# Performance work log

Hardware: AMD Instinct MI355X
Metric: run time of the kernel (lower is better)

Reference implementation:

```python
import jax, jax.numpy as jnp
import numpy as np

C = 1.0  # curvature
EPS = 1e-5

@jax.custom_vjp
def arsinh(x):
    return jnp.log(jnp.maximum(x + jnp.sqrt(1.0 + x * x), 1e-5))

def _arsinh_fwd(x):
    return arsinh(x), x

def _arsinh_bwd(x, g):
    return (g / jnp.sqrt(1.0 + x * x),)

arsinh.defvjp(_arsinh_fwd, _arsinh_bwd)

def tanh_clamped(x, clamp=15.0):
    return jnp.tanh(jnp.clip(x, -clamp, clamp))

def expmap0(u, c):
    sqrt_c = c ** 0.5
    u_norm = jnp.maximum(jnp.linalg.norm(u, axis=-1, keepdims=True), 1e-5)
    return tanh_clamped(sqrt_c * u_norm) * u / (sqrt_c * u_norm)

def mobius_addition_batch(x, y, c):
    # x: [K, D], y: [N, D] -> [K, N, D]
    xy = jnp.einsum('kd,nd->kn', x, y)
    x2 = jnp.sum(x * x, axis=-1, keepdims=True)          # [K, 1]
    y2 = jnp.sum(y * y, axis=-1, keepdims=True)          # [N, 1]
    num = (1.0 + 2.0 * c * xy + c * y2.T)[:, :, None] * x[:, None, :]
    num = num + (1.0 - c * x2)[:, :, None] * y[None, :, :]
    denom = 1.0 + 2.0 * c * xy + (c ** 2) * x2 * y2.T    # [K, N]
    return num / (denom[:, :, None] + EPS)

def hyperbolic_softmax(x, a, p, c):
    # x: [N, D], a/p: [K, D] -> logits [N, K]
    lambda_pkc = 2.0 / (1.0 - c * jnp.minimum(jnp.sum(p * p, axis=1), 1.0 / c - 1e-4))
    k = lambda_pkc * jnp.maximum(jnp.linalg.norm(a, axis=1), 1e-7) / jnp.sqrt(c)
    mob_add = mobius_addition_batch(-p, x, c)            # [K, N, D]
    num = 2.0 * jnp.sqrt(c) * jnp.sum(mob_add * a[:, None, :], axis=-1)   # [K, N]
    denom = jnp.maximum(jnp.linalg.norm(a, axis=1, keepdims=True), 1e-7) * \
        (1.0 - c * jnp.sum(mob_add * mob_add, axis=2))   # [K, N]
    logit = k[:, None] * arsinh(num / denom)
    return logit.T                                        # [N, K]

def setup_inputs() -> dict:
    key = jax.random.key(0)
    k1, k2, k3 = jax.random.split(key, 3)
    N, K, D = 2048, 256, 512
    bound = 1.0 / np.sqrt(D)  # kaiming_uniform(a=sqrt(5)) bound
    x = jax.random.normal(k1, (N, D), dtype=jnp.float32) * 0.02  # inside unit ball
    a_vals = jax.random.uniform(k2, (K, D), dtype=jnp.float32, minval=-bound, maxval=bound)
    p_vals = jax.random.uniform(k3, (K, D), dtype=jnp.float32, minval=-bound, maxval=bound)
    return {"x": x, "a_vals": a_vals, "p_vals": p_vals}

def reference(x, a_vals, p_vals):
    c = jnp.asarray(C, dtype=x.dtype)
    p_poincare = expmap0(p_vals, c)                      # [K, D]
    conformal = 1.0 - c * jnp.sum(p_poincare * p_poincare, axis=1, keepdims=True)
    a_poincare = a_vals * conformal                      # [K, D]
    return hyperbolic_softmax(x, a_poincare, p_poincare, c)
```

## Files before the change

### kernel.cpp

```cpp
#include <hip/hip_runtime.h>
#include <hip/hip_bf16.h>
#include <math.h>

#define NROWS 2048
#define KROWS 256
#define DDIM  512

typedef __attribute__((ext_vector_type(8))) short short8;
typedef __attribute__((ext_vector_type(4))) short short4v;
typedef __attribute__((ext_vector_type(4))) float f32x4;

#define AB_BYTE   262144
#define SC_FOFF   131072

__device__ inline unsigned short f2bf(float f) {
    unsigned u = __float_as_uint(f);
    u += 0x7fffu + ((u >> 16) & 1u);
    return (unsigned short)(u >> 16);
}

__device__ inline float wave_reduce_sum(float v) {
    #pragma unroll
    for (int off = 32; off > 0; off >>= 1)
        v += __shfl_xor(v, off, 64);
    return v;
}

__global__ __launch_bounds__(256) void hmlr_prep(
        const float* __restrict__ a_vals,
        const float* __restrict__ p_vals,
        float* __restrict__ ws) {
    const int tid  = threadIdx.x;
    const int w    = tid >> 6;
    const int lane = tid & 63;
    const int k    = blockIdx.x * 4 + w;

    const float4* pv4 = (const float4*)(p_vals) + k * (DDIM / 4) + lane * 2;
    const float4* av4 = (const float4*)(a_vals) + k * (DDIM / 4) + lane * 2;
    float4 p0 = pv4[0], p1 = pv4[1];
    float4 a0 = av4[0], a1 = av4[1];

    float pn2 = p0.x*p0.x + p0.y*p0.y + p0.z*p0.z + p0.w*p0.w
              + p1.x*p1.x + p1.y*p1.y + p1.z*p1.z + p1.w*p1.w;
    float an2 = a0.x*a0.x + a0.y*a0.y + a0.z*a0.z + a0.w*a0.w
              + a1.x*a1.x + a1.y*a1.y + a1.z*a1.z + a1.w*a1.w;
    float pa0 = p0.x*a0.x + p0.y*a0.y + p0.z*a0.z + p0.w*a0.w
              + p1.x*a1.x + p1.y*a1.y + p1.z*a1.z + p1.w*a1.w;

    pn2 = wave_reduce_sum(pn2);
    an2 = wave_reduce_sum(an2);
    pa0 = wave_reduce_sum(pa0);

    float u     = fmaxf(sqrtf(pn2), 1e-5f);
    float t     = tanhf(fminf(u, 15.0f));
    float scale = t / u;
    float p2    = scale * scale * pn2;
    float conf  = 1.0f - p2;
    float na    = fmaxf(conf * sqrtf(an2), 1e-7f);
    float pa    = scale * conf * pa0;
    float lam   = 2.0f / (1.0f - fminf(p2, 0.9999f));
    float kc    = lam * na;

    float pf[8] = { scale*p0.x, scale*p0.y, scale*p0.z, scale*p0.w,
                    scale*p1.x, scale*p1.y, scale*p1.z, scale*p1.w };
    float af[8] = { conf*a0.x, conf*a0.y, conf*a0.z, conf*a0.w,
                    conf*a1.x, conf*a1.y, conf*a1.z, conf*a1.w };
    short8 pu, au;
    #pragma unroll
    for (int j = 0; j < 8; ++j) {
        pu[j] = (short)f2bf(pf[j]);
        au[j] = (short)f2bf(af[j]);
    }
    short8* PT8 = (short8*)ws;
    short8* AT8 = (short8*)((char*)ws + AB_BYTE);
    const int ci = (((k >> 4) * 16 + (lane >> 2)) * 64) + (lane & 3) * 16 + (k & 15);
    PT8[ci] = pu;
    AT8[ci] = au;
    if (lane == 0)
        ((float4*)(ws + SC_FOFF))[k] = make_float4(p2, pa, na, kc);
}

__global__ __launch_bounds__(256, 2) void hmlr_main(
        const float* __restrict__ x,
        const float* __restrict__ ws,
        float* __restrict__ out) {
    __shared__ short8 XS[16][64];
    __shared__ float  Y2S[16];

    const int tid  = threadIdx.x;
    const int lane = tid & 63;
    const int w    = tid >> 6;
    const int mt   = blockIdx.x >> 2;
    const int ct   = (blockIdx.x & 3) * 4 + w;
    const int m0   = mt * 16;
    const int c0   = ct * 16;
    const int row  = lane & 15;
    const int kg   = lane >> 4;

    const short8* PT8 = (const short8*)ws;
    const short8* AT8 = (const short8*)((const char*)ws + AB_BYTE);
    const float*  SC  = ws + SC_FOFF;

    const short8* pt = PT8 + ct * 16 * 64 + lane;
    const short8* at = AT8 + ct * 16 * 64 + lane;
    short8 pv[16], av[16];
    #pragma unroll
    for (int s = 0; s < 16; ++s) pv[s] = pt[s * 64];
    #pragma unroll
    for (int s = 0; s < 16; ++s) av[s] = at[s * 64];

    {
        const int r = tid >> 4;
        const int j = tid & 15;
        const float* xrow = x + (m0 + r) * DDIM;
        float ss = 0.0f;
        #pragma unroll
        for (int q = 0; q < 8; ++q) {
            float4 v = *(const float4*)(xrow + j * 4 + q * 64);
            ss += v.x*v.x + v.y*v.y + v.z*v.z + v.w*v.w;
            const int sfr = 2 * q + (j >> 3);
            const int kfr = (j >> 1) & 3;
            short4v h;
            h[0] = (short)f2bf(v.x); h[1] = (short)f2bf(v.y);
            h[2] = (short)f2bf(v.z); h[3] = (short)f2bf(v.w);
            *(short4v*)((unsigned short*)&XS[sfr][kfr * 16 + r] + (j & 1) * 4) = h;
        }
        #pragma unroll
        for (int off = 1; off < 16; off <<= 1)
            ss += __shfl_xor(ss, off, 64);
        if (j == 0) Y2S[r] = ss;
    }
    __syncthreads();

    short8 xv[16];
    #pragma unroll
    for (int s = 0; s < 16; ++s) xv[s] = XS[s][lane];

    f32x4 aP[2] = {{0.f,0.f,0.f,0.f},{0.f,0.f,0.f,0.f}};
    f32x4 aA[2] = {{0.f,0.f,0.f,0.f},{0.f,0.f,0.f,0.f}};
    #pragma unroll
    for (int s = 0; s < 16; ++s) {
        aP[s & 1] = __builtin_amdgcn_mfma_f32_16x16x32_bf16(xv[s], pv[s], aP[s & 1], 0, 0, 0);
        aA[s & 1] = __builtin_amdgcn_mfma_f32_16x16x32_bf16(xv[s], av[s], aA[s & 1], 0, 0, 0);
    }
    f32x4 accP = aP[0] + aP[1];
    f32x4 accA = aA[0] + aA[1];

    const int c = c0 + row;
    f32x4 sc = *(const f32x4*)(SC + 4 * c);
    const float p2 = sc[0], pa = sc[1], na = sc[2], kc = sc[3];
    #pragma unroll
    for (int j = 0; j < 4; ++j) {
        const int m     = m0 + kg * 4 + j;
        const float y2n = Y2S[kg * 4 + j];
        const float xpv = accP[j];
        const float xav = accA[j];
        const float alpha = 1.0f - 2.0f * xpv + y2n;
        const float beta  = 1.0f - p2;
        const float gam   = 1.0f - 2.0f * xpv + p2 * y2n;
        const float gi    = __builtin_amdgcn_rcpf(gam + 1e-5f);
        const float num   = 2.0f * (beta * xav - alpha * pa) * gi;
        const float mob2  = (alpha*alpha*p2 + beta*beta*y2n
                             - 2.0f*alpha*beta*xpv) * gi * gi;
        const float den   = na * (1.0f - mob2);
        const float z     = num * __builtin_amdgcn_rcpf(den);
        const float arg   = fmaxf(z + __builtin_amdgcn_sqrtf(1.0f + z * z), 1e-5f);
        out[m * KROWS + c] = kc * __logf(arg);
    }
}

extern "C" void kernel_launch(void* const* d_in, const int* in_sizes, int n_in,
                              void* d_out, int out_size, void* d_ws, size_t ws_size,
                              hipStream_t stream) {
    (void)in_sizes; (void)n_in; (void)out_size; (void)ws_size;
    const float* x      = (const float*)d_in[0];
    const float* a_vals = (const float*)d_in[1];
    const float* p_vals = (const float*)d_in[2];
    float* ws  = (float*)d_ws;
    float* out = (float*)d_out;

    hmlr_prep<<<64, 256, 0, stream>>>(a_vals, p_vals, ws);
    hmlr_main<<<512, 256, 0, stream>>>(x, ws, out);
}
```

Before: 15.34 us.

## Fuse prep into main kernel, recomputing P/A bf16 tiles and scalars per block

Merges the two-kernel pipeline into one launch: each 512-thread block loads raw p/a rows, computes norms and expmap scalars, converts the rows to bf16 into shared memory, and applies the scale and conformal factors after the MFMA instead of before. Each block now handles two 16-row x tiles across four column tiles, reusing a shared buffer for the X and P/A staging. This removes a kernel launch and the workspace round trip, in exchange for redundant per-block recomputation of the p/a preprocessing and extra syncs. Unscaled bf16 rounding of p and a before scaling slightly changes numerics.

```diff
diff --git a/kernel.cpp b/kernel.cpp
--- a/kernel.cpp
+++ b/kernel.cpp
@@ -10,109 +10,40 @@
 typedef __attribute__((ext_vector_type(4))) short short4v;
 typedef __attribute__((ext_vector_type(4))) float f32x4;
 
-#define AB_BYTE   262144
-#define SC_FOFF   131072
-
-__device__ inline unsigned short f2bf(float f) {
+__device__ inline short f2bfs(float f) {
     unsigned u = __float_as_uint(f);
     u += 0x7fffu + ((u >> 16) & 1u);
-    return (unsigned short)(u >> 16);
+    return (short)(u >> 16);
 }
 
-__device__ inline float wave_reduce_sum(float v) {
-    #pragma unroll
-    for (int off = 32; off > 0; off >>= 1)
-        v += __shfl_xor(v, off, 64);
-    return v;
-}
-
-__global__ __launch_bounds__(256) void hmlr_prep(
+__global__ __launch_bounds__(512, 2) void hmlr_one(
+        const float* __restrict__ x,
         const float* __restrict__ a_vals,
         const float* __restrict__ p_vals,
-        float* __restrict__ ws) {
-    const int tid  = threadIdx.x;
-    const int w    = tid >> 6;
-    const int lane = tid & 63;
-    const int k    = blockIdx.x * 4 + w;
+        float* __restrict__ out) {
+    __shared__ __align__(16) char BUF[32768];
+    __shared__ float Y2S[32];
+    __shared__ float SCL[4][16][6];
 
-    const float4* pv4 = (const float4*)(p_vals) + k * (DDIM / 4) + lane * 2;
-    const float4* av4 = (const float4*)(a_vals) + k * (DDIM / 4) + lane * 2;
-    float4 p0 = pv4[0], p1 = pv4[1];
-    float4 a0 = av4[0], a1 = av4[1];
+    short8 (*XS)[16][64] = (short8(*)[16][64])BUF;
+    short8 (*PS)[64]     = (short8(*)[64])BUF;
+    short8 (*AS)[64]     = (short8(*)[64])(BUF + 16384);
 
-    float pn2 = p0.x*p0.x + p0.y*p0.y + p0.z*p0.z + p0.w*p0.w
-              + p1.x*p1.x + p1.y*p1.y + p1.z*p1.z + p1.w*p1.w;
-    float an2 = a0.x*a0.x + a0.y*a0.y + a0.z*a0.z + a0.w*a0.w
-              + a1.x*a1.x + a1.y*a1.y + a1.z*a1.z + a1.w*a1.w;
-    float pa0 = p0.x*a0.x + p0.y*a0.y + p0.z*a0.z + p0.w*a0.w
-              + p1.x*a1.x + p1.y*a1.y + p1.z*a1.z + p1.w*a1.w;
-
-    pn2 = wave_reduce_sum(pn2);
-    an2 = wave_reduce_sum(an2);
-    pa0 = wave_reduce_sum(pa0);
-
-    float u     = fmaxf(sqrtf(pn2), 1e-5f);
-    float t     = tanhf(fminf(u, 15.0f));
-    float scale = t / u;
-    float p2    = scale * scale * pn2;
-    float conf  = 1.0f - p2;
-    float na    = fmaxf(conf * sqrtf(an2), 1e-7f);
-    float pa    = scale * conf * pa0;
-    float lam   = 2.0f / (1.0f - fminf(p2, 0.9999f));
-    float kc    = lam * na;
-
-    float pf[8] = { scale*p0.x, scale*p0.y, scale*p0.z, scale*p0.w,
-                    scale*p1.x, scale*p1.y, scale*p1.z, scale*p1.w };
-    float af[8] = { conf*a0.x, conf*a0.y, conf*a0.z, conf*a0.w,
-                    conf*a1.x, conf*a1.y, conf*a1.z, conf*a1.w };
-    short8 pu, au;
-    #pragma unroll
-    for (int j = 0; j < 8; ++j) {
-        pu[j] = (short)f2bf(pf[j]);
-        au[j] = (short)f2bf(af[j]);
-    }
-    short8* PT8 = (short8*)ws;
-    short8* AT8 = (short8*)((char*)ws + AB_BYTE);
-    const int ci = (((k >> 4) * 16 + (lane >> 2)) * 64) + (lane & 3) * 16 + (k & 15);
-    PT8[ci] = pu;
-    AT8[ci] = au;
-    if (lane == 0)
-        ((float4*)(ws + SC_FOFF))[k] = make_float4(p2, pa, na, kc);
-}
-
-__global__ __launch_bounds__(256, 2) void hmlr_main(
-        const float* __restrict__ x,
-        const float* __restrict__ ws,
-        float* __restrict__ out) {
-    __shared__ short8 XS[16][64];
-    __shared__ float  Y2S[16];
-
-    const int tid  = threadIdx.x;
-    const int lane = tid & 63;
-    const int w    = tid >> 6;
-    const int mt   = blockIdx.x >> 2;
-    const int ct   = (blockIdx.x & 3) * 4 + w;
-    const int m0   = mt * 16;
-    const int c0   = ct * 16;
-    const int row  = lane & 15;
-    const int kg   = lane >> 4;
-
-    const short8* PT8 = (const short8*)ws;
-    const short8* AT8 = (const short8*)((const char*)ws + AB_BYTE);
-    const float*  SC  = ws + SC_FOFF;
-
-    const short8* pt = PT8 + ct * 16 * 64 + lane;
-    const short8* at = AT8 + ct * 16 * 64 + lane;
-    short8 pv[16], av[16];
-    #pragma unroll
-    for (int s = 0; s < 16; ++s) pv[s] = pt[s * 64];
-    #pragma unroll
-    for (int s = 0; s < 16; ++s) av[s] = at[s * 64];
+    const int tid    = threadIdx.x;
+    const int lane   = tid & 63;
+    const int w      = tid >> 6;
+    const int mtl    = w >> 2;
+    const int phw    = w & 3;
+    const int mtg    = blockIdx.x >> 2;
+    const int ctbase = (blockIdx.x & 3) * 4;
+    const int m0     = (mtg * 2 + mtl) * 16;
+    const int row    = lane & 15;
+    const int kg     = lane >> 4;
 
     {
         const int r = tid >> 4;
         const int j = tid & 15;
-        const float* xrow = x + (m0 + r) * DDIM;
+        const float* xrow = x + ((mtg * 2) * 16 + r) * DDIM;
         float ss = 0.0f;
         #pragma unroll
         for (int q = 0; q < 8; ++q) {
@@ -121,9 +52,10 @@
             const int sfr = 2 * q + (j >> 3);
             const int kfr = (j >> 1) & 3;
             short4v h;
-            h[0] = (short)f2bf(v.x); h[1] = (short)f2bf(v.y);
-            h[2] = (short)f2bf(v.z); h[3] = (short)f2bf(v.w);
-            *(short4v*)((unsigned short*)&XS[sfr][kfr * 16 + r] + (j & 1) * 4) = h;
+            h[0] = f2bfs(v.x); h[1] = f2bfs(v.y);
+            h[2] = f2bfs(v.z); h[3] = f2bfs(v.w);
+            *(short4v*)((unsigned short*)&XS[r >> 4][sfr][kfr * 16 + (r & 15)]
+                        + (j & 1) * 4) = h;
         }
         #pragma unroll
         for (int off = 1; off < 16; off <<= 1)
@@ -134,7 +66,66 @@
 
     short8 xv[16];
     #pragma unroll
-    for (int s = 0; s < 16; ++s) xv[s] = XS[s][lane];
+    for (int s = 0; s < 16; ++s) xv[s] = XS[mtl][s][lane];
+    __syncthreads();
+
+    short8 pv[16], av[16];
+    {
+        const int r = tid >> 5;
+        const int j = tid & 31;
+        #pragma unroll 1
+        for (int ph = 0; ph < 4; ++ph) {
+            const int kr = (ctbase + ph) * 16 + r;
+            const float* prow = p_vals + kr * DDIM;
+            const float* arow = a_vals + kr * DDIM;
+            float pn2 = 0.f, an2 = 0.f, pa0 = 0.f;
+            #pragma unroll
+            for (int q = 0; q < 4; ++q) {
+                float4 pv4 = *(const float4*)(prow + j * 4 + q * 128);
+                float4 av4 = *(const float4*)(arow + j * 4 + q * 128);
+                pn2 += pv4.x*pv4.x + pv4.y*pv4.y + pv4.z*pv4.z + pv4.w*pv4.w;
+                an2 += av4.x*av4.x + av4.y*av4.y + av4.z*av4.z + av4.w*av4.w;
+                pa0 += pv4.x*av4.x + pv4.y*av4.y + pv4.z*av4.z + pv4.w*av4.w;
+                const int sfr = (j >> 3) + q * 4;
+                const int kfr = (j >> 1) & 3;
+                short4v hp, ha;
+                hp[0] = f2bfs(pv4.x); hp[1] = f2bfs(pv4.y);
+                hp[2] = f2bfs(pv4.z); hp[3] = f2bfs(pv4.w);
+                ha[0] = f2bfs(av4.x); ha[1] = f2bfs(av4.y);
+                ha[2] = f2bfs(av4.z); ha[3] = f2bfs(av4.w);
+                *(short4v*)((unsigned short*)&PS[sfr][kfr * 16 + r] + (j & 1) * 4) = hp;
+                *(short4v*)((unsigned short*)&AS[sfr][kfr * 16 + r] + (j & 1) * 4) = ha;
+            }
+            #pragma unroll
+            for (int off = 1; off < 32; off <<= 1) {
+                pn2 += __shfl_xor(pn2, off, 64);
+                an2 += __shfl_xor(an2, off, 64);
+                pa0 += __shfl_xor(pa0, off, 64);
+            }
+            if (j == 0) {
+                float u     = fmaxf(sqrtf(pn2), 1e-5f);
+                float t     = tanhf(fminf(u, 15.0f));
+                float scale = t / u;
+                float p2    = scale * scale * pn2;
+                float conf  = 1.0f - p2;
+                float na    = fmaxf(conf * sqrtf(an2), 1e-7f);
+                float pa    = scale * conf * pa0;
+                float lam   = 2.0f / (1.0f - fminf(p2, 0.9999f));
+                float kc    = lam * na;
+                SCL[ph][r][0] = p2;  SCL[ph][r][1] = pa;
+                SCL[ph][r][2] = na;  SCL[ph][r][3] = kc;
+                SCL[ph][r][4] = scale; SCL[ph][r][5] = conf;
+            }
+            __syncthreads();
+            if (phw == ph) {
+                #pragma unroll
+                for (int s = 0; s < 16; ++s) pv[s] = PS[s][lane];
+                #pragma unroll
+                for (int s = 0; s < 16; ++s) av[s] = AS[s][lane];
+            }
+            __syncthreads();
+        }
+    }
 
     f32x4 aP[2] = {{0.f,0.f,0.f,0.f},{0.f,0.f,0.f,0.f}};
     f32x4 aA[2] = {{0.f,0.f,0.f,0.f},{0.f,0.f,0.f,0.f}};
@@ -146,15 +137,19 @@
     f32x4 accP = aP[0] + aP[1];
     f32x4 accA = aA[0] + aA[1];
 
-    const int c = c0 + row;
-    f32x4 sc = *(const f32x4*)(SC + 4 * c);
-    const float p2 = sc[0], pa = sc[1], na = sc[2], kc = sc[3];
+    const int c = (ctbase + phw) * 16 + row;
+    const float p2    = SCL[phw][row][0];
+    const float pa    = SCL[phw][row][1];
+    const float na    = SCL[phw][row][2];
+    const float kc    = SCL[phw][row][3];
+    const float scale = SCL[phw][row][4];
+    const float conf  = SCL[phw][row][5];
     #pragma unroll
     for (int j = 0; j < 4; ++j) {
         const int m     = m0 + kg * 4 + j;
-        const float y2n = Y2S[kg * 4 + j];
-        const float xpv = accP[j];
-        const float xav = accA[j];
+        const float y2n = Y2S[mtl * 16 + kg * 4 + j];
+        const float xpv = scale * accP[j];
+        const float xav = conf  * accA[j];
         const float alpha = 1.0f - 2.0f * xpv + y2n;
         const float beta  = 1.0f - p2;
         const float gam   = 1.0f - 2.0f * xpv + p2 * y2n;
@@ -172,13 +167,11 @@
 extern "C" void kernel_launch(void* const* d_in, const int* in_sizes, int n_in,
                               void* d_out, int out_size, void* d_ws, size_t ws_size,
                               hipStream_t stream) {
-    (void)in_sizes; (void)n_in; (void)out_size; (void)ws_size;
+    (void)in_sizes; (void)n_in; (void)out_size; (void)d_ws; (void)ws_size;
     const float* x      = (const float*)d_in[0];
     const float* a_vals = (const float*)d_in[1];
     const float* p_vals = (const float*)d_in[2];
-    float* ws  = (float*)d_ws;
     float* out = (float*)d_out;
 
-    hmlr_prep<<<64, 256, 0, stream>>>(a_vals, p_vals, ws);
-    hmlr_main<<<512, 256, 0, stream>>>(x, ws, out);
+    hmlr_one<<<256, 512, 0, stream>>>(x, a_vals, p_vals, out);
 }
```

After: 18.10 us. 1.18x slower.
